# Kernel tuning notes

Hardware: AMD Instinct MI355X
Metric: run time of the kernel (lower is better)

The kernel has to match this reference:

```python
import jax, jax.numpy as jnp
import numpy as np

H_DIM = 128
EMB = 16
MODES = 6
TRAJ = MODES * 2  # 12
PRED_LEN = 30
B = 65536
NEG_SLOPE = 0.01  # F.leaky_relu default


def setup_inputs() -> dict:
    key = jax.random.key(0)
    ks = jax.random.split(key, 16)
    s = lambda k, shape, fan_in: jax.random.uniform(k, shape, jnp.float32, -1.0, 1.0) / np.sqrt(fan_in)
    return {
        "last_obs": jax.random.normal(ks[0], (B, 2), jnp.float32),
        "last_obs_rel": jax.random.normal(ks[1], (B, 2), jnp.float32),
        "h0": jax.random.normal(ks[2], (1, B, H_DIM), jnp.float32),
        "c0": jax.random.normal(ks[3], (1, B, H_DIM), jnp.float32),
        # nn.LSTM(EMB, H_DIM, 1): weight_ih (4H, EMB), weight_hh (4H, H), biases (4H,)
        "W_ih": s(ks[4], (4 * H_DIM, EMB), H_DIM),
        "W_hh": s(ks[5], (4 * H_DIM, H_DIM), H_DIM),
        "b_ih": s(ks[6], (4 * H_DIM,), H_DIM),
        "b_hh": s(ks[7], (4 * H_DIM,), H_DIM),
        # spatial_embedding: Linear(TRAJ, EMB)
        "W_emb": s(ks[8], (EMB, TRAJ), TRAJ),
        "b_emb": s(ks[9], (EMB,), TRAJ),
        # hidden2pos: Linear(H_DIM, TRAJ)
        "W_pos": s(ks[10], (TRAJ, H_DIM), H_DIM),
        "b_pos": s(ks[11], (TRAJ,), H_DIM),
        # confidences: Linear(H_DIM, MODES)
        "W_conf": s(ks[12], (MODES, H_DIM), H_DIM),
        "b_conf": s(ks[13], (MODES,), H_DIM),
    }


def _lstm_cell(x, h, c, W_ih, W_hh, b):
    # x: (B, EMB), h/c: (B, H). PyTorch gate order: i, f, g, o
    gates = x @ W_ih.T + h @ W_hh.T + b  # (B, 4H)
    i, f, g, o = jnp.split(gates, 4, axis=-1)
    c_new = jax.nn.sigmoid(f) * c + jax.nn.sigmoid(i) * jnp.tanh(g)
    h_new = jax.nn.sigmoid(o) * jnp.tanh(c_new)
    return h_new, c_new


def reference(last_obs, last_obs_rel, h0, c0, W_ih, W_hh, b_ih, b_hh,
              W_emb, b_emb, W_pos, b_pos, W_conf, b_conf):
    b_gate = b_ih + b_hh
    batch = last_obs_rel.shape[0]
    # repeat_interleave last_obs_rel over modes -> (B, 12)
    rel0 = jnp.repeat(last_obs_rel[:, None, :], MODES, axis=1).reshape(batch, TRAJ)
    dec_in = jax.nn.leaky_relu(rel0 @ W_emb.T + b_emb, NEG_SLOPE)  # (B, EMB); eval mode => no dropout

    def step(carry, _):
        h, c, x = carry
        h, c = _lstm_cell(x, h, c, W_ih, W_hh, b_gate)
        rel_pos = h @ W_pos.T + b_pos                                # (B, TRAJ)
        x_next = jax.nn.leaky_relu(rel_pos @ W_emb.T + b_emb, NEG_SLOPE)
        return (h, c, x_next), rel_pos

    (_, _, _), rels = jax.lax.scan(step, (h0[0], c0[0], dec_in), None, length=PRED_LEN)
    # rels: (PRED_LEN, B, TRAJ) -> (B, MODES, PRED_LEN, 2)
    pred = rels.reshape(PRED_LEN, batch, MODES, 2).transpose(1, 2, 0, 3)
    # conf uses the ORIGINAL (un-updated) state_tuple_h, as in the source
    conf = jax.nn.softmax(h0[0] @ W_conf.T + b_conf, axis=1)         # (B, MODES)
    return pred, conf
```

## Files before the change

kernel.cpp:

```cpp
#include <hip/hip_runtime.h>

typedef _Float16 f16;
typedef f16 f16x8 __attribute__((ext_vector_type(8)));
typedef float f32x4 __attribute__((ext_vector_type(4)));

#define MT 64
#define NSTEP 30

__device__ __forceinline__ float fast_sigmoid(float x) {
    float e = __expf(-x);
    return __builtin_amdgcn_rcpf(1.0f + e);
}
__device__ __forceinline__ float fast_tanh(float x) {
    float e = __expf(2.0f * x);
    return 1.0f - 2.0f * __builtin_amdgcn_rcpf(1.0f + e);
}

__global__ __launch_bounds__(512) void mdlstm_kernel(
    const float* __restrict__ lor,
    const float* __restrict__ h0,
    const float* __restrict__ c0,
    const float* __restrict__ W_ih,
    const float* __restrict__ W_hh,
    const float* __restrict__ b_ih, const float* __restrict__ b_hh,
    const float* __restrict__ W_emb,
    const float* __restrict__ b_emb,
    const float* __restrict__ W_pos,
    const float* __restrict__ b_pos,
    const float* __restrict__ W_conf,
    const float* __restrict__ b_conf,
    float* __restrict__ out, int batch)
{
    __shared__ f16 h_lds[2 * MT * 128];
    __shared__ f16 x_lds[MT * 16];
    __shared__ f16 rel_lds[MT * 16];

    const int tid = threadIdx.x;
    const int wv  = tid >> 6;
    const int ln  = tid & 63;
    const int g   = ln >> 4;
    const int q   = ln & 15;
    const int b0  = blockIdx.x * MT;
    if (b0 >= batch) return;

    f16x8 whh[4][4];
    #pragma unroll
    for (int g4 = 0; g4 < 4; ++g4) {
        const int col = g4 * 128 + wv * 16 + q;
        #pragma unroll
        for (int kf = 0; kf < 4; ++kf) {
            const float* p = W_hh + col * 128 + kf * 32 + g * 8;
            f16x8 v;
            #pragma unroll
            for (int j = 0; j < 8; ++j) v[j] = (f16)p[j];
            whh[g4][kf] = v;
        }
    }
    f16x8 wih[4];
    #pragma unroll
    for (int g4 = 0; g4 < 4; ++g4) {
        const int col = g4 * 128 + wv * 16 + q;
        f16x8 v = {};
        if (g < 2) {
            const float* p = W_ih + col * 16 + g * 8;
            #pragma unroll
            for (int j = 0; j < 8; ++j) v[j] = (f16)p[j];
        }
        wih[g4] = v;
    }
    float bg[4];
    #pragma unroll
    for (int g4 = 0; g4 < 4; ++g4) {
        const int col = g4 * 128 + wv * 16 + q;
        bg[g4] = b_ih[col] + b_hh[col];
    }
    f16x8 wpos[4];
    #pragma unroll
    for (int kf = 0; kf < 4; ++kf) {
        f16x8 v = {};
        if (q < 12) {
            const float* p = W_pos + q * 128 + kf * 32 + g * 8;
            #pragma unroll
            for (int j = 0; j < 8; ++j) v[j] = (f16)p[j];
        }
        wpos[kf] = v;
    }
    const float bpos = (q < 12) ? b_pos[q] : 0.0f;
    f16x8 wemb = {};
    #pragma unroll
    for (int j = 0; j < 8; ++j) {
        const int k = g * 8 + j;
        if (k < 12) wemb[j] = (f16)W_emb[q * 12 + k];
    }
    const float bemb = b_emb[q];

    f32x4 c_st[4];
    #pragma unroll
    for (int mt = 0; mt < 4; ++mt)
        #pragma unroll
        for (int r = 0; r < 4; ++r)
            c_st[mt][r] = c0[(b0 + mt * 16 + g * 4 + r) * 128 + wv * 16 + q];

    {
        const int row = tid >> 3;
        const int seg = tid & 7;
        const float* p = h0 + (b0 + row) * 128 + seg * 16;
        #pragma unroll
        for (int half = 0; half < 2; ++half) {
            f16x8 v;
            #pragma unroll
            for (int j = 0; j < 8; ++j) v[j] = (f16)p[half * 8 + j];
            const int chunk = seg * 2 + half;
            *(f16x8*)&h_lds[row * 128 + ((chunk ^ (row & 7)) << 3)] = v;
        }
    }

    if (wv < 4) {
        const int mt = wv;
        const int m  = mt * 16 + q;
        const float lx = lor[(b0 + m) * 2 + 0];
        const float ly = lor[(b0 + m) * 2 + 1];
        f16x8 rf = {};
        #pragma unroll
        for (int j = 0; j < 8; ++j) {
            const int k = g * 8 + j;
            if (k < 12) rf[j] = (f16)((j & 1) ? ly : lx);
        }
        f32x4 xacc = {bemb, bemb, bemb, bemb};
        xacc = __builtin_amdgcn_mfma_f32_16x16x32_f16(rf, wemb, xacc, 0, 0, 0);
        #pragma unroll
        for (int r = 0; r < 4; ++r) {
            float xv = xacc[r];
            xv = fmaxf(xv, 0.01f * xv);
            x_lds[(mt * 16 + g * 4 + r) * 16 + q] = (f16)xv;
        }
    }

    {
        const int e  = tid >> 3;
        const int p8 = tid & 7;
        const float* hp = h0 + (b0 + e) * 128 + p8 * 16;
        float pc[6];
        #pragma unroll
        for (int md = 0; md < 6; ++md) {
            const float* wc = W_conf + md * 128 + p8 * 16;
            float s = 0.f;
            #pragma unroll
            for (int i = 0; i < 16; ++i) s += hp[i] * wc[i];
            pc[md] = s;
        }
        #pragma unroll
        for (int md = 0; md < 6; ++md) {
            pc[md] += __shfl_down(pc[md], 4, 8);
            pc[md] += __shfl_down(pc[md], 2, 8);
            pc[md] += __shfl_down(pc[md], 1, 8);
        }
        if (p8 == 0) {
            float mx = -1e30f;
            #pragma unroll
            for (int md = 0; md < 6; ++md) { pc[md] += b_conf[md]; mx = fmaxf(mx, pc[md]); }
            float s = 0.f;
            #pragma unroll
            for (int md = 0; md < 6; ++md) { pc[md] = __expf(pc[md] - mx); s += pc[md]; }
            const float rs = __builtin_amdgcn_rcpf(s);
            float* cp = out + batch * 360 + (b0 + e) * 6;
            #pragma unroll
            for (int md = 0; md < 6; ++md) cp[md] = pc[md] * rs;
        }
    }

    __syncthreads();

    int buf = 0;
    for (int t = 0; t < NSTEP; ++t) {
        const int hbase_r = buf * (MT * 128);
        const int hbase_w = (buf ^ 1) * (MT * 128);
        #pragma unroll
        for (int mt = 0; mt < 4; ++mt) {
            const int row = mt * 16 + q;
            f16x8 hf[4];
            #pragma unroll
            for (int kf = 0; kf < 4; ++kf)
                hf[kf] = *(const f16x8*)&h_lds[hbase_r + row * 128 + (((4 * kf + g) ^ (row & 7)) << 3)];
            f16x8 xf = {};
            if (g < 2) xf = *(const f16x8*)&x_lds[row * 16 + g * 8];
            f32x4 acc[4];
            #pragma unroll
            for (int g4 = 0; g4 < 4; ++g4) {
                f32x4 a = {bg[g4], bg[g4], bg[g4], bg[g4]};
                #pragma unroll
                for (int kf = 0; kf < 4; ++kf)
                    a = __builtin_amdgcn_mfma_f32_16x16x32_f16(hf[kf], whh[g4][kf], a, 0, 0, 0);
                a = __builtin_amdgcn_mfma_f32_16x16x32_f16(xf, wih[g4], a, 0, 0, 0);
                acc[g4] = a;
            }
            #pragma unroll
            for (int r = 0; r < 4; ++r) {
                const float iv = fast_sigmoid(acc[0][r]);
                const float fv = fast_sigmoid(acc[1][r]);
                const float gv = fast_tanh(acc[2][r]);
                const float ov = fast_sigmoid(acc[3][r]);
                const float cv = fv * c_st[mt][r] + iv * gv;
                c_st[mt][r] = cv;
                const float hv = ov * fast_tanh(cv);
                const int wrow = mt * 16 + g * 4 + r;
                const int k = wv * 16 + q;
                h_lds[hbase_w + wrow * 128 + (((k >> 3) ^ (wrow & 7)) << 3) + (k & 7)] = (f16)hv;
            }
        }
        __syncthreads();

        if (wv < 4) {
            const int mt = wv;
            const int row = mt * 16 + q;
            f16x8 hf[4];
            #pragma unroll
            for (int kf = 0; kf < 4; ++kf)
                hf[kf] = *(const f16x8*)&h_lds[hbase_w + row * 128 + (((4 * kf + g) ^ (row & 7)) << 3)];
            f32x4 racc = {bpos, bpos, bpos, bpos};
            #pragma unroll
            for (int kf = 0; kf < 4; ++kf)
                racc = __builtin_amdgcn_mfma_f32_16x16x32_f16(hf[kf], wpos[kf], racc, 0, 0, 0);
            #pragma unroll
            for (int r = 0; r < 4; ++r) {
                const int m = mt * 16 + g * 4 + r;
                if (q < 12)
                    out[(b0 + m) * 360 + (q >> 1) * 60 + t * 2 + (q & 1)] = racc[r];
                rel_lds[m * 16 + q] = (f16)racc[r];
            }
            __threadfence_block();
            f16x8 rf = {};
            if (g < 2) rf = *(const f16x8*)&rel_lds[row * 16 + g * 8];
            f32x4 xacc = {bemb, bemb, bemb, bemb};
            xacc = __builtin_amdgcn_mfma_f32_16x16x32_f16(rf, wemb, xacc, 0, 0, 0);
            #pragma unroll
            for (int r = 0; r < 4; ++r) {
                float xv = xacc[r];
                xv = fmaxf(xv, 0.01f * xv);
                x_lds[(mt * 16 + g * 4 + r) * 16 + q] = (f16)xv;
            }
        }
        buf ^= 1;
        __syncthreads();
    }
}

extern "C" void kernel_launch(void* const* d_in, const int* in_sizes, int n_in,
                              void* d_out, int out_size, void* d_ws, size_t ws_size,
                              hipStream_t stream) {
    const float* last_obs_rel = (const float*)d_in[1];
    const float* h0     = (const float*)d_in[2];
    const float* c0     = (const float*)d_in[3];
    const float* W_ih   = (const float*)d_in[4];
    const float* W_hh   = (const float*)d_in[5];
    const float* b_ih   = (const float*)d_in[6];
    const float* b_hh   = (const float*)d_in[7];
    const float* W_emb  = (const float*)d_in[8];
    const float* b_emb  = (const float*)d_in[9];
    const float* W_pos  = (const float*)d_in[10];
    const float* b_pos  = (const float*)d_in[11];
    const float* W_conf = (const float*)d_in[12];
    const float* b_conf = (const float*)d_in[13];
    float* out = (float*)d_out;

    const int batch = in_sizes[1] / 2;
    const int grid  = (batch + MT - 1) / MT;
    mdlstm_kernel<<<grid, 512, 0, stream>>>(last_obs_rel, h0, c0, W_ih, W_hh,
                                            b_ih, b_hh, W_emb, b_emb, W_pos,
                                            b_pos, W_conf, b_conf, out, batch);
}
```

Measured before the change: 527.4 us.

## Fold gate scaling and bias into MFMA weights, transpose operands, pack stores

Pre-scales the LSTM weights by -log2e or 2·log2e so the gate nonlinearities become raw exp2 calls. The gate bias is folded into the input MFMA through a constant-one lane, and sigmoid·tanh products are merged so each needs a single reciprocal. The MFMA operands are swapped so each lane owns four contiguous output columns, which allows packed f16x4 LDS writes of h, x and rel, and vectorised c0 loads and output stores. W_pos moves to LDS to free registers, and the time loop is unrolled by two to drop the buffer index arithmetic. Folding the bias into f16 weights and clamping tanh's input change precision slightly.

```diff
diff --git a/kernel.cpp b/kernel.cpp
--- a/kernel.cpp
+++ b/kernel.cpp
@@ -1,19 +1,32 @@
 #include <hip/hip_runtime.h>
 
 typedef _Float16 f16;
+typedef f16 f16x2 __attribute__((ext_vector_type(2)));
+typedef f16 f16x4 __attribute__((ext_vector_type(4)));
 typedef f16 f16x8 __attribute__((ext_vector_type(8)));
 typedef float f32x4 __attribute__((ext_vector_type(4)));
+typedef __fp16 fp16x2_raw __attribute__((ext_vector_type(2)));
 
 #define MT 64
 #define NSTEP 30
-
-__device__ __forceinline__ float fast_sigmoid(float x) {
-    float e = __expf(-x);
-    return __builtin_amdgcn_rcpf(1.0f + e);
-}
-__device__ __forceinline__ float fast_tanh(float x) {
-    float e = __expf(2.0f * x);
-    return 1.0f - 2.0f * __builtin_amdgcn_rcpf(1.0f + e);
+#define LOG2E 1.4426950408889634f
+
+__device__ __forceinline__ float rcp_f(float x) { return __builtin_amdgcn_rcpf(x); }
+__device__ __forceinline__ float exp2_f(float x) {
+#if __has_builtin(__builtin_amdgcn_exp2f)
+    return __builtin_amdgcn_exp2f(x);
+#else
+    return __builtin_exp2f(x);
+#endif
+}
+__device__ __forceinline__ f16x2 pk2(float a, float b) {
+    fp16x2_raw t = __builtin_amdgcn_cvt_pkrtz(a, b);
+    return __builtin_bit_cast(f16x2, t);
+}
+__device__ __forceinline__ f16x4 pk4(float a, float b, float c, float d) {
+    f16x2 lo = pk2(a, b), hi = pk2(c, d);
+    f16x4 r; r[0] = lo[0]; r[1] = lo[1]; r[2] = hi[0]; r[3] = hi[1];
+    return r;
 }
 
 __global__ __launch_bounds__(512) void mdlstm_kernel(
@@ -34,6 +47,12 @@
     __shared__ f16 h_lds[2 * MT * 128];
     __shared__ f16 x_lds[MT * 16];
     __shared__ f16 rel_lds[MT * 16];
+    __shared__ f16 wpos_lds[4 * 64 * 8];
+
+    char* hb   = (char*)h_lds;
+    char* xb   = (char*)x_lds;
+    char* relb = (char*)rel_lds;
+    char* wpb  = (char*)wpos_lds;
 
     const int tid = threadIdx.x;
     const int wv  = tid >> 6;
@@ -43,6 +62,8 @@
     const int b0  = blockIdx.x * MT;
     if (b0 >= batch) return;
 
+    const float gsc[4] = {-LOG2E, -LOG2E, 2.f * LOG2E, -LOG2E};
+
     f16x8 whh[4][4];
     #pragma unroll
     for (int g4 = 0; g4 < 4; ++g4) {
@@ -52,7 +73,7 @@
             const float* p = W_hh + col * 128 + kf * 32 + g * 8;
             f16x8 v;
             #pragma unroll
-            for (int j = 0; j < 8; ++j) v[j] = (f16)p[j];
+            for (int j = 0; j < 8; ++j) v[j] = (f16)(p[j] * gsc[g4]);
             whh[g4][kf] = v;
         }
     }
@@ -64,82 +85,88 @@
         if (g < 2) {
             const float* p = W_ih + col * 16 + g * 8;
             #pragma unroll
-            for (int j = 0; j < 8; ++j) v[j] = (f16)p[j];
+            for (int j = 0; j < 8; ++j) v[j] = (f16)(p[j] * gsc[g4]);
+        } else if (g == 2) {
+            v[0] = (f16)((b_ih[col] + b_hh[col]) * gsc[g4]);
         }
         wih[g4] = v;
     }
-    float bg[4];
-    #pragma unroll
-    for (int g4 = 0; g4 < 4; ++g4) {
-        const int col = g4 * 128 + wv * 16 + q;
-        bg[g4] = b_ih[col] + b_hh[col];
-    }
-    f16x8 wpos[4];
-    #pragma unroll
-    for (int kf = 0; kf < 4; ++kf) {
-        f16x8 v = {};
-        if (q < 12) {
-            const float* p = W_pos + q * 128 + kf * 32 + g * 8;
-            #pragma unroll
-            for (int j = 0; j < 8; ++j) v[j] = (f16)p[j];
-        }
-        wpos[kf] = v;
-    }
-    const float bpos = (q < 12) ? b_pos[q] : 0.0f;
     f16x8 wemb = {};
     #pragma unroll
     for (int j = 0; j < 8; ++j) {
         const int k = g * 8 + j;
         if (k < 12) wemb[j] = (f16)W_emb[q * 12 + k];
     }
-    const float bemb = b_emb[q];
+    f32x4 bembv, bposv;
+    #pragma unroll
+    for (int r = 0; r < 4; ++r) {
+        bembv[r] = b_emb[4 * g + r];
+        bposv[r] = (4 * g + r < 12) ? b_pos[4 * g + r] : 0.f;
+    }
+
+    if (wv == 0) {
+        #pragma unroll
+        for (int kf = 0; kf < 4; ++kf) {
+            f16x8 v = {};
+            if (q < 12) {
+                const float* p = W_pos + q * 128 + kf * 32 + g * 8;
+                #pragma unroll
+                for (int j = 0; j < 8; ++j) v[j] = (f16)p[j];
+            }
+            *(f16x8*)(wpb + kf * 1024 + ln * 16) = v;
+        }
+    }
 
     f32x4 c_st[4];
     #pragma unroll
     for (int mt = 0; mt < 4; ++mt)
-        #pragma unroll
-        for (int r = 0; r < 4; ++r)
-            c_st[mt][r] = c0[(b0 + mt * 16 + g * 4 + r) * 128 + wv * 16 + q];
+        c_st[mt] = *(const f32x4*)(c0 + (size_t)(b0 + 16 * mt + q) * 128 + 16 * wv + 4 * g);
+
+    const int swz = (q & 7) << 5;
+    int rdbase[4];
+    #pragma unroll
+    for (int kf = 0; kf < 4; ++kf) rdbase[kf] = q * 256 + ((kf * 64 + g * 16) ^ swz);
+    const int wrb = q * 256 + ((wv * 32 + g * 8) ^ swz);
+    const int xrd = q * 32 + g * 16;
+    const int xwr = q * 32 + g * 8;
+
+    float* outp = out + (size_t)(b0 + 16 * wv + q) * 360 + 2 * g * 60;
 
     {
-        const int row = tid >> 3;
-        const int seg = tid & 7;
-        const float* p = h0 + (b0 + row) * 128 + seg * 16;
-        #pragma unroll
-        for (int half = 0; half < 2; ++half) {
+        const int row = tid >> 3, seg = tid & 7;
+        const float* p = h0 + (size_t)(b0 + row) * 128 + seg * 16;
+        const int rswz = (row & 7) << 5;
+        #pragma unroll
+        for (int hh = 0; hh < 2; ++hh) {
             f16x8 v;
             #pragma unroll
-            for (int j = 0; j < 8; ++j) v[j] = (f16)p[half * 8 + j];
-            const int chunk = seg * 2 + half;
-            *(f16x8*)&h_lds[row * 128 + ((chunk ^ (row & 7)) << 3)] = v;
+            for (int j = 0; j < 8; ++j) v[j] = (f16)p[hh * 8 + j];
+            const int off = row * 256 + (((seg * 4 + 2 * hh) * 8) ^ rswz);
+            *(f16x8*)(hb + off) = v;
         }
     }
 
     if (wv < 4) {
-        const int mt = wv;
-        const int m  = mt * 16 + q;
-        const float lx = lor[(b0 + m) * 2 + 0];
-        const float ly = lor[(b0 + m) * 2 + 1];
+        const float2 xy = *(const float2*)(lor + (size_t)(b0 + 16 * wv + q) * 2);
         f16x8 rf = {};
-        #pragma unroll
-        for (int j = 0; j < 8; ++j) {
-            const int k = g * 8 + j;
-            if (k < 12) rf[j] = (f16)((j & 1) ? ly : lx);
-        }
-        f32x4 xacc = {bemb, bemb, bemb, bemb};
-        xacc = __builtin_amdgcn_mfma_f32_16x16x32_f16(rf, wemb, xacc, 0, 0, 0);
-        #pragma unroll
-        for (int r = 0; r < 4; ++r) {
-            float xv = xacc[r];
-            xv = fmaxf(xv, 0.01f * xv);
-            x_lds[(mt * 16 + g * 4 + r) * 16 + q] = (f16)xv;
-        }
+        if (g < 2) {
+            #pragma unroll
+            for (int j = 0; j < 8; ++j) {
+                const int k = g * 8 + j;
+                if (k < 12) rf[j] = (f16)((k & 1) ? xy.y : xy.x);
+            }
+        }
+        f32x4 xacc = bembv;
+        xacc = __builtin_amdgcn_mfma_f32_16x16x32_f16(wemb, rf, xacc, 0, 0, 0);
+        f16x4 xp = pk4(fmaxf(xacc[0], .01f * xacc[0]), fmaxf(xacc[1], .01f * xacc[1]),
+                       fmaxf(xacc[2], .01f * xacc[2]), fmaxf(xacc[3], .01f * xacc[3]));
+        *(f16x4*)(xb + wv * 512 + xwr) = xp;
     }
 
     {
         const int e  = tid >> 3;
         const int p8 = tid & 7;
-        const float* hp = h0 + (b0 + e) * 128 + p8 * 16;
+        const float* hp = h0 + (size_t)(b0 + e) * 128 + p8 * 16;
         float pc[6];
         #pragma unroll
         for (int md = 0; md < 6; ++md) {
@@ -162,8 +189,8 @@
             float s = 0.f;
             #pragma unroll
             for (int md = 0; md < 6; ++md) { pc[md] = __expf(pc[md] - mx); s += pc[md]; }
-            const float rs = __builtin_amdgcn_rcpf(s);
-            float* cp = out + batch * 360 + (b0 + e) * 6;
+            const float rs = rcp_f(s);
+            float* cp = out + (size_t)batch * 360 + (size_t)(b0 + e) * 6;
             #pragma unroll
             for (int md = 0; md < 6; ++md) cp[md] = pc[md] * rs;
         }
@@ -171,78 +198,78 @@
 
     __syncthreads();
 
-    int buf = 0;
-    for (int t = 0; t < NSTEP; ++t) {
-        const int hbase_r = buf * (MT * 128);
-        const int hbase_w = (buf ^ 1) * (MT * 128);
-        #pragma unroll
-        for (int mt = 0; mt < 4; ++mt) {
-            const int row = mt * 16 + q;
-            f16x8 hf[4];
-            #pragma unroll
-            for (int kf = 0; kf < 4; ++kf)
-                hf[kf] = *(const f16x8*)&h_lds[hbase_r + row * 128 + (((4 * kf + g) ^ (row & 7)) << 3)];
-            f16x8 xf = {};
-            if (g < 2) xf = *(const f16x8*)&x_lds[row * 16 + g * 8];
-            f32x4 acc[4];
-            #pragma unroll
-            for (int g4 = 0; g4 < 4; ++g4) {
-                f32x4 a = {bg[g4], bg[g4], bg[g4], bg[g4]};
-                #pragma unroll
-                for (int kf = 0; kf < 4; ++kf)
-                    a = __builtin_amdgcn_mfma_f32_16x16x32_f16(hf[kf], whh[g4][kf], a, 0, 0, 0);
-                a = __builtin_amdgcn_mfma_f32_16x16x32_f16(xf, wih[g4], a, 0, 0, 0);
-                acc[g4] = a;
-            }
-            #pragma unroll
-            for (int r = 0; r < 4; ++r) {
-                const float iv = fast_sigmoid(acc[0][r]);
-                const float fv = fast_sigmoid(acc[1][r]);
-                const float gv = fast_tanh(acc[2][r]);
-                const float ov = fast_sigmoid(acc[3][r]);
-                const float cv = fv * c_st[mt][r] + iv * gv;
-                c_st[mt][r] = cv;
-                const float hv = ov * fast_tanh(cv);
-                const int wrow = mt * 16 + g * 4 + r;
-                const int k = wv * 16 + q;
-                h_lds[hbase_w + wrow * 128 + (((k >> 3) ^ (wrow & 7)) << 3) + (k & 7)] = (f16)hv;
-            }
-        }
-        __syncthreads();
-
-        if (wv < 4) {
-            const int mt = wv;
-            const int row = mt * 16 + q;
-            f16x8 hf[4];
-            #pragma unroll
-            for (int kf = 0; kf < 4; ++kf)
-                hf[kf] = *(const f16x8*)&h_lds[hbase_w + row * 128 + (((4 * kf + g) ^ (row & 7)) << 3)];
-            f32x4 racc = {bpos, bpos, bpos, bpos};
-            #pragma unroll
-            for (int kf = 0; kf < 4; ++kf)
-                racc = __builtin_amdgcn_mfma_f32_16x16x32_f16(hf[kf], wpos[kf], racc, 0, 0, 0);
-            #pragma unroll
-            for (int r = 0; r < 4; ++r) {
-                const int m = mt * 16 + g * 4 + r;
-                if (q < 12)
-                    out[(b0 + m) * 360 + (q >> 1) * 60 + t * 2 + (q & 1)] = racc[r];
-                rel_lds[m * 16 + q] = (f16)racc[r];
-            }
-            __threadfence_block();
-            f16x8 rf = {};
-            if (g < 2) rf = *(const f16x8*)&rel_lds[row * 16 + g * 8];
-            f32x4 xacc = {bemb, bemb, bemb, bemb};
-            xacc = __builtin_amdgcn_mfma_f32_16x16x32_f16(rf, wemb, xacc, 0, 0, 0);
-            #pragma unroll
-            for (int r = 0; r < 4; ++r) {
-                float xv = xacc[r];
-                xv = fmaxf(xv, 0.01f * xv);
-                x_lds[(mt * 16 + g * 4 + r) * 16 + q] = (f16)xv;
-            }
-        }
-        buf ^= 1;
-        __syncthreads();
-    }
+#define STEP(BR, BW, T_) do {                                                   \
+    _Pragma("unroll")                                                           \
+    for (int mt = 0; mt < 4; ++mt) {                                            \
+        f32x4 a0 = {0,0,0,0}, a1 = {0,0,0,0}, a2 = {0,0,0,0}, a3 = {0,0,0,0};   \
+        _Pragma("unroll")                                                       \
+        for (int kf = 0; kf < 4; ++kf) {                                        \
+            f16x8 hf = *(const f16x8*)(hb + (BR) + mt * 4096 + rdbase[kf]);     \
+            a0 = __builtin_amdgcn_mfma_f32_16x16x32_f16(whh[0][kf], hf, a0, 0, 0, 0); \
+            a1 = __builtin_amdgcn_mfma_f32_16x16x32_f16(whh[1][kf], hf, a1, 0, 0, 0); \
+            a2 = __builtin_amdgcn_mfma_f32_16x16x32_f16(whh[2][kf], hf, a2, 0, 0, 0); \
+            a3 = __builtin_amdgcn_mfma_f32_16x16x32_f16(whh[3][kf], hf, a3, 0, 0, 0); \
+        }                                                                       \
+        {                                                                       \
+            f16x8 xf = {};                                                      \
+            if (g < 2)       xf = *(const f16x8*)(xb + mt * 512 + xrd);         \
+            else if (g == 2) xf[0] = (f16)1.f;                                  \
+            a0 = __builtin_amdgcn_mfma_f32_16x16x32_f16(wih[0], xf, a0, 0, 0, 0); \
+            a1 = __builtin_amdgcn_mfma_f32_16x16x32_f16(wih[1], xf, a1, 0, 0, 0); \
+            a2 = __builtin_amdgcn_mfma_f32_16x16x32_f16(wih[2], xf, a2, 0, 0, 0); \
+            a3 = __builtin_amdgcn_mfma_f32_16x16x32_f16(wih[3], xf, a3, 0, 0, 0); \
+        }                                                                       \
+        f32x4 hv;                                                               \
+        _Pragma("unroll")                                                       \
+        for (int r = 0; r < 4; ++r) {                                           \
+            const float ei = exp2_f(a0[r]);                                     \
+            const float ef = exp2_f(a1[r]);                                     \
+            const float eg = exp2_f(a2[r]);                                     \
+            const float eo = exp2_f(a3[r]);                                     \
+            const float sf  = rcp_f(1.f + ef);                                  \
+            const float itg = (eg - 1.f) * rcp_f((1.f + ei) * (1.f + eg));      \
+            const float cv  = sf * c_st[mt][r] + itg;                           \
+            c_st[mt][r] = cv;                                                   \
+            const float ec = exp2_f(fminf(cv, 30.f) * (2.f * LOG2E));           \
+            hv[r] = (ec - 1.f) * rcp_f((1.f + eo) * (1.f + ec));                \
+        }                                                                       \
+        *(f16x4*)(hb + (BW) + mt * 4096 + wrb) = pk4(hv[0], hv[1], hv[2], hv[3]); \
+    }                                                                           \
+    __syncthreads();                                            \
+    if (wv < 4) {                                                               \
+        f32x4 racc = bposv;                                                     \
+        _Pragma("unroll")                                                       \
+        for (int kf = 0; kf < 4; ++kf) {                                        \
+            f16x8 wp = *(const f16x8*)(wpb + kf * 1024 + ln * 16);              \
+            f16x8 hf = *(const f16x8*)(hb + (BW) + wv * 4096 + rdbase[kf]);     \
+            racc = __builtin_amdgcn_mfma_f32_16x16x32_f16(wp, hf, racc, 0, 0, 0); \
+        }                                                                       \
+        if (g < 3) {                                                            \
+            float2 s0 = {racc[0], racc[1]};                                     \
+            float2 s1 = {racc[2], racc[3]};                                     \
+            float* pp = outp + 2 * (T_);                                        \
+            *(float2*)pp = s0;                                                  \
+            *(float2*)(pp + 60) = s1;                                           \
+        }                                                                       \
+        *(f16x4*)(relb + wv * 512 + xwr) = pk4(racc[0], racc[1], racc[2], racc[3]); \
+        __threadfence_block();                                                  \
+        f16x8 rf = {};                                                          \
+        if (g < 2) rf = *(const f16x8*)(relb + wv * 512 + xrd);                 \
+        f32x4 xacc = bembv;                                                     \
+        xacc = __builtin_amdgcn_mfma_f32_16x16x32_f16(wemb, rf, xacc, 0, 0, 0); \
+        f16x4 xp = pk4(fmaxf(xacc[0], .01f * xacc[0]), fmaxf(xacc[1], .01f * xacc[1]), \
+                       fmaxf(xacc[2], .01f * xacc[2]), fmaxf(xacc[3], .01f * xacc[3])); \
+        *(f16x4*)(xb + wv * 512 + xwr) = xp;                                    \
+    }                                                                           \
+    __syncthreads();                                          \
+} while (0)
+
+    #pragma unroll 1
+    for (int tt = 0; tt < NSTEP; tt += 2) {
+        STEP(0, 16384, tt);
+        STEP(16384, 0, tt + 1);
+    }
+#undef STEP
 }
 
 extern "C" void kernel_launch(void* const* d_in, const int* in_sizes, int n_in,
```

Measured after the change: 461.1 us. 1.14x faster.
